# Performance work log

Measured on AMD Instinct MI355X. Metric: run time of the kernel, lower is better.

The kernel has to match this reference:

```python
import jax, jax.numpy as jnp
import numpy as np

B, T = 64, 512
IN, OUT, H = 256, 256, 1024


def _lstm_cell(x, h, c, Wih, Whh, bih, bhh):
    # PyTorch LSTMCell: gates = x@Wih^T + bih + h@Whh^T + bhh, order i,f,g,o
    gates = x @ Wih.T + bih + h @ Whh.T + bhh
    i, f, g, o = jnp.split(gates, 4, axis=-1)
    c_new = jax.nn.sigmoid(f) * c + jax.nn.sigmoid(i) * jnp.tanh(g)
    h_new = jax.nn.sigmoid(o) * jnp.tanh(c_new)
    return h_new, c_new


def setup_inputs() -> dict:
    key = jax.random.key(0)
    ks = jax.random.split(key, 12)
    s = 1.0 / np.sqrt(H)  # torch default uniform(-1/sqrt(H), 1/sqrt(H))
    u = lambda k, shp: jax.random.uniform(k, shp, jnp.float32, -s, s)
    return {
        "z": jax.random.normal(ks[0], (B, H), jnp.float32),
        "x": jax.random.normal(ks[1], (B, T, IN), jnp.float32),
        "Wih0": u(ks[2], (4 * H, IN)),
        "Whh0": u(ks[3], (4 * H, H)),
        "bih0": u(ks[4], (4 * H,)),
        "bhh0": u(ks[5], (4 * H,)),
        "Wih1": u(ks[6], (4 * H, H)),
        "Whh1": u(ks[7], (4 * H, H)),
        "bih1": u(ks[8], (4 * H,)),
        "bhh1": u(ks[9], (4 * H,)),
        "Wlin": u(ks[10], (OUT, H)),
        "blin": u(ks[11], (OUT,)),
    }


def reference(z, x, Wih0, Whh0, bih0, bhh0, Wih1, Whh1, bih1, bhh1, Wlin, blin):
    # Teacher-forcing unroll: h_t[l] init to z, c_t[l] init to 0, first input is zeros,
    # then input at step t+1 is x[:, t].
    x_tb = jnp.swapaxes(x, 0, 1)  # [T, B, IN]
    c0_init = jnp.zeros_like(z)

    def step(carry, x_t):
        cur_in, h0, c0, h1, c1 = carry
        h0, c0 = _lstm_cell(cur_in, h0, c0, Wih0, Whh0, bih0, bhh0)
        h1, c1 = _lstm_cell(h0, h1, c1, Wih1, Whh1, bih1, bhh1)
        out_t = h1 @ Wlin.T + blin  # [B, OUT]
        return (x_t, h0, c0, h1, c1), out_t

    init = (jnp.zeros((z.shape[0], Wih0.shape[1]), z.dtype), z, c0_init, z, c0_init)
    _, outs = jax.lax.scan(step, init, x_tb)  # outs: [T, B, OUT]
    return jnp.swapaxes(outs, 0, 1)  # [B, T, OUT]
```

## Files before the change

kernel.cpp:

```cpp
#include <hip/hip_runtime.h>
#include <hip/hip_bf16.h>
#include <math.h>


typedef __attribute__((ext_vector_type(8))) short bf16x8;
typedef __attribute__((ext_vector_type(4))) float f32x4;
typedef unsigned long long u64;

__device__ __forceinline__ float sigm(float v) { return 1.f / (1.f + expf(-v)); }

__device__ __forceinline__ unsigned short bf16_bits(float v) {
  __hip_bfloat16 hb = __float2bfloat16(v);
  unsigned short us;
  __builtin_memcpy(&us, &hb, 2);
  return us;
}

__device__ __forceinline__ void vstore_bf16(__hip_bfloat16* p, float v) {
  *(volatile unsigned short*)p = bf16_bits(v);
}


__global__ __launch_bounds__(256) void prep_w0(const float* __restrict__ Wih0,
                                               const float* __restrict__ Whh0,
                                               __hip_bfloat16* __restrict__ W0) {
  const unsigned n = 4096u * 1280u;
  for (unsigned d = blockIdx.x * blockDim.x + threadIdx.x; d < n;
       d += blockDim.x * gridDim.x) {
    unsigned r = d / 1280u;
    unsigned k = d - r * 1280u;
    unsigned u = r >> 2, g = r & 3u;
    unsigned srow = g * 1024u + u;
    float v = (k < 256u) ? Wih0[(size_t)srow * 256u + k]
                         : Whh0[(size_t)srow * 1024u + (k - 256u)];
    W0[d] = __float2bfloat16(v);
  }
}

__global__ __launch_bounds__(256) void prep_w1(const float* __restrict__ Wih1,
                                               const float* __restrict__ Whh1,
                                               const float* __restrict__ Wlin,
                                               __hip_bfloat16* __restrict__ W1) {
  const unsigned n = 4352u * 2048u;
  for (unsigned d = blockIdx.x * blockDim.x + threadIdx.x; d < n;
       d += blockDim.x * gridDim.x) {
    unsigned r = d >> 11;
    unsigned k = d & 2047u;
    float v;
    if (r < 4096u) {
      unsigned u = r >> 2, g = r & 3u;
      unsigned srow = g * 1024u + u;
      v = (k < 1024u) ? Wih1[(size_t)srow * 1024u + k]
                      : Whh1[(size_t)srow * 1024u + (k - 1024u)];
    } else {
      unsigned o = r - 4096u;
      v = (k < 1024u) ? 0.f : Wlin[(size_t)o * 1024u + (k - 1024u)];
    }
    W1[d] = __float2bfloat16(v);
  }
}

__global__ __launch_bounds__(256) void prep_x(const float* __restrict__ x,
                                              __hip_bfloat16* __restrict__ xbf) {
  const unsigned n = 512u * 64u * 256u;
  for (unsigned d = blockIdx.x * blockDim.x + threadIdx.x; d < n;
       d += blockDim.x * gridDim.x) {
    unsigned t = d >> 14;
    unsigned b = (d >> 8) & 63u;
    unsigned k = d & 255u;
    float v = (t == 0u) ? 0.f : x[((size_t)b * 512u + (t - 1u)) * 256u + k];
    xbf[d] = __float2bfloat16(v);
  }
}

__global__ __launch_bounds__(256) void prep_misc(
    const float* __restrict__ bih0, const float* __restrict__ bhh0,
    const float* __restrict__ bih1, const float* __restrict__ bhh1,
    const float* __restrict__ z, float* __restrict__ b0, float* __restrict__ b1,
    __hip_bfloat16* __restrict__ h0buf, __hip_bfloat16* __restrict__ h1buf) {
  for (int i = blockIdx.x * blockDim.x + threadIdx.x; i < 73728;
       i += blockDim.x * gridDim.x) {
    if (i < 4096) {
      int u = i >> 2, g = i & 3;
      b0[i] = bih0[g * 1024 + u] + bhh0[g * 1024 + u];
    } else if (i < 8192) {
      int r = i - 4096;
      int u = r >> 2, g = r & 3;
      b1[r] = bih1[g * 1024 + u] + bhh1[g * 1024 + u];
    } else {
      int j = i - 8192;
      float zv = z[j];
      vstore_bf16(h0buf + j, zv);
      vstore_bf16(h1buf + 2 * 65536 + j, zv);
    }
  }
}


__device__ __forceinline__ void do_proj(const __hip_bfloat16* __restrict__ h1p,
                                        const bf16x8* wp, float (*red)[16][68],
                                        const float* __restrict__ blin,
                                        float* __restrict__ out, int pcol,
                                        int pbat, int t_out, int tid, int w,
                                        int col, int kq) {
  f32x4 a0 = {0.f, 0.f, 0.f, 0.f};
  const __hip_bfloat16* ab =
      h1p + ((size_t)((pbat << 4) + col) << 10) + (w << 7) + (kq << 3);
#pragma unroll
  for (int c = 0; c < 4; ++c) {
    bf16x8 f = *(const bf16x8*)(ab + (c << 5));
    a0 = __builtin_amdgcn_mfma_f32_16x16x32_bf16(f, wp[c], a0, 0, 0, 0);
  }
  *(f32x4*)&red[w][col][(kq << 2)] = a0;
  __syncthreads();
  if (tid < 256) {
    int o_l = tid & 15, b = tid >> 4;
    float v = blin[(pcol << 4) + o_l];
#pragma unroll
    for (int ww = 0; ww < 8; ++ww) v += red[ww][o_l][b];
    out[(((size_t)((pbat << 4) + b) << 9) + (size_t)t_out) * 256 + (pcol << 4) +
        o_l] = v;
  }
}


__global__ __launch_bounds__(512) void k_persist(
    const __hip_bfloat16* __restrict__ xbf, const __hip_bfloat16* __restrict__ W0,
    const __hip_bfloat16* __restrict__ W1, const float* __restrict__ b0,
    const float* __restrict__ b1, const float* __restrict__ blin,
    __hip_bfloat16* __restrict__ h0buf, __hip_bfloat16* __restrict__ h1buf,
    float* __restrict__ out, unsigned* __restrict__ flags) {
  const int tid = threadIdx.x;
  const int lane = tid & 63;
  const int w = tid >> 6;
  const int bid = blockIdx.x;
  const int cb = bid << 4;
  const int col = lane & 15;
  const int kq = lane >> 4;
  const int n = cb + col;
  const bool isproj = (bid < 64);
  const int pcol = bid & 15;
  const int pbat = (bid >> 4) & 3;

  __shared__ int s_lead;
  {
    unsigned* lead = flags + 256;
    if (tid == 0) {
      unsigned xcc = 0;
      asm volatile("s_getreg_b32 %0, hwreg(HW_REG_XCC_ID)" : "=s"(xcc));
      unsigned old = __hip_atomic_fetch_add(&lead[xcc & 7u], 1u,
                                            __ATOMIC_RELAXED,
                                            __HIP_MEMORY_SCOPE_AGENT);
      s_lead = (old == 0u || bid < 8) ? 1 : 0;
    }
  }

  bf16x8 wa[5], wb[8], wp[4];
  {
    const __hip_bfloat16* p = W0 + (size_t)n * 1280 + w * 160 + (kq << 3);
#pragma unroll
    for (int c = 0; c < 5; ++c) wa[c] = *(const bf16x8*)(p + (c << 5));
  }
  {
    const __hip_bfloat16* p = W1 + ((size_t)n << 11) + (w << 8) + (kq << 3);
#pragma unroll
    for (int c = 0; c < 8; ++c) wb[c] = *(const bf16x8*)(p + (c << 5));
  }
  if (isproj) {
    const __hip_bfloat16* p = W1 +
        ((size_t)(4096 + (pcol << 4) + col) << 11) + 1024 + (w << 7) + (kq << 3);
#pragma unroll
    for (int c = 0; c < 4; ++c) wp[c] = *(const bf16x8*)(p + (c << 5));
  }

  const int u_l = tid & 3, bq = tid >> 2;
  float bias0[4], bias1[4];
  if (tid < 256) {
#pragma unroll
    for (int g = 0; g < 4; ++g) {
      bias0[g] = b0[cb + (u_l << 2) + g];
      bias1[g] = b1[cb + (u_l << 2) + g];
    }
  }
  float c0v = 0.f, c1v = 0.f;

  __shared__ float red[8][16][68];
  __shared__ unsigned short hst0[64][4];
  __shared__ unsigned short hst1[64][4];

  __syncthreads();

  for (int t = 0; t < 512; ++t) {
    const __hip_bfloat16* h0prev = h0buf + ((size_t)(t & 1) << 16);
    const __hip_bfloat16* h0cur = h0buf + ((size_t)((t + 1) & 1) << 16);
    const __hip_bfloat16* h1prev = h1buf + ((size_t)((t + 2) % 3) << 16);

    {
      f32x4 a0 = {0.f, 0.f, 0.f, 0.f}, a1 = a0, a2 = a0, a3 = a0;
#pragma unroll
      for (int c = 0; c < 5; ++c) {
        const int k0 = w * 160 + (c << 5);
        const __hip_bfloat16* ab;
        size_t rs;
        if (k0 < 256) {
          ab = xbf + ((size_t)t << 14) + k0 + (kq << 3);
          rs = 256;
        } else {
          ab = h0prev + (k0 - 256) + (kq << 3);
          rs = 1024;
        }
        bf16x8 f0 = *(const bf16x8*)(ab + (size_t)col * rs);
        bf16x8 f1 = *(const bf16x8*)(ab + (size_t)(16 + col) * rs);
        bf16x8 f2 = *(const bf16x8*)(ab + (size_t)(32 + col) * rs);
        bf16x8 f3 = *(const bf16x8*)(ab + (size_t)(48 + col) * rs);
        a0 = __builtin_amdgcn_mfma_f32_16x16x32_bf16(f0, wa[c], a0, 0, 0, 0);
        a1 = __builtin_amdgcn_mfma_f32_16x16x32_bf16(f1, wa[c], a1, 0, 0, 0);
        a2 = __builtin_amdgcn_mfma_f32_16x16x32_bf16(f2, wa[c], a2, 0, 0, 0);
        a3 = __builtin_amdgcn_mfma_f32_16x16x32_bf16(f3, wa[c], a3, 0, 0, 0);
      }
      *(f32x4*)&red[w][col][(kq << 2)] = a0;
      *(f32x4*)&red[w][col][16 + (kq << 2)] = a1;
      *(f32x4*)&red[w][col][32 + (kq << 2)] = a2;
      *(f32x4*)&red[w][col][48 + (kq << 2)] = a3;
    }
    __syncthreads();
    if (tid < 256) {
      float gg[4];
#pragma unroll
      for (int g = 0; g < 4; ++g) {
        float v = bias0[g];
#pragma unroll
        for (int ww = 0; ww < 8; ++ww) v += red[ww][(u_l << 2) + g][bq];
        gg[g] = v;
      }
      float cn = sigm(gg[1]) * c0v + sigm(gg[0]) * tanhf(gg[2]);
      c0v = cn;
      hst0[bq][u_l] = bf16_bits(sigm(gg[3]) * tanhf(cn));
    }
    __syncthreads();

    if (w == 0) {
      __builtin_amdgcn_s_waitcnt(0);
      if (s_lead) {
        __builtin_amdgcn_fence(__ATOMIC_ACQUIRE, "agent");
      } else {
        __builtin_amdgcn_sched_barrier(0);
        asm volatile("buffer_inv" ::: "memory");
        __builtin_amdgcn_sched_barrier(0);
      }
      u64 v0;
      __builtin_memcpy(&v0, &hst0[lane][0], 8);
      __hip_atomic_store((u64*)(h0buf + (((size_t)((t + 1) & 1)) << 16) +
                                ((size_t)lane << 10) + (cb >> 2)),
                         v0, __ATOMIC_RELAXED, __HIP_MEMORY_SCOPE_AGENT);
      if (t > 0) {
        u64 v1;
        __builtin_memcpy(&v1, &hst1[lane][0], 8);
        __hip_atomic_store((u64*)(h1buf + (((size_t)((t + 2) % 3)) << 16) +
                                  ((size_t)lane << 10) + (cb >> 2)),
                           v1, __ATOMIC_RELAXED, __HIP_MEMORY_SCOPE_AGENT);
      }
      __builtin_amdgcn_s_waitcnt(0);
      __builtin_amdgcn_sched_barrier(0);
      if (lane == 0)
        __hip_atomic_store(&flags[bid], (unsigned)(t + 1), __ATOMIC_RELAXED,
                           __HIP_MEMORY_SCOPE_AGENT);
    }

    if (isproj && t >= 2)
      do_proj(h1buf + (((size_t)((t + 1) % 3)) << 16), wp, red, blin, out,
              pcol, pbat, t - 2, tid, w, col, kq);

    if (w == 0) {
      const unsigned tgt = (unsigned)(t + 1);
      const u64* fq = (const u64*)flags;
      for (;;) {
        u64 q0 = __hip_atomic_load(&fq[2 * lane], __ATOMIC_RELAXED,
                                   __HIP_MEMORY_SCOPE_AGENT);
        u64 q1 = __hip_atomic_load(&fq[2 * lane + 1], __ATOMIC_RELAXED,
                                   __HIP_MEMORY_SCOPE_AGENT);
        int ok = ((unsigned)q0 >= tgt) & ((unsigned)(q0 >> 32) >= tgt) &
                 ((unsigned)q1 >= tgt) & ((unsigned)(q1 >> 32) >= tgt);
        if (__all(ok)) break;
        __builtin_amdgcn_s_sleep(1);
      }
    }
    __syncthreads();

    {
      const __hip_bfloat16* ab =
          ((w < 4) ? h0cur : h1prev) + ((w & 3) << 8) + (kq << 3);
      f32x4 a0 = {0.f, 0.f, 0.f, 0.f}, a1 = a0, a2 = a0, a3 = a0;
#pragma unroll
      for (int c = 0; c < 8; ++c) {
        const __hip_bfloat16* p = ab + (c << 5);
        bf16x8 f0 = *(const bf16x8*)(p + ((size_t)col << 10));
        bf16x8 f1 = *(const bf16x8*)(p + ((size_t)(16 + col) << 10));
        bf16x8 f2 = *(const bf16x8*)(p + ((size_t)(32 + col) << 10));
        bf16x8 f3 = *(const bf16x8*)(p + ((size_t)(48 + col) << 10));
        a0 = __builtin_amdgcn_mfma_f32_16x16x32_bf16(f0, wb[c], a0, 0, 0, 0);
        a1 = __builtin_amdgcn_mfma_f32_16x16x32_bf16(f1, wb[c], a1, 0, 0, 0);
        a2 = __builtin_amdgcn_mfma_f32_16x16x32_bf16(f2, wb[c], a2, 0, 0, 0);
        a3 = __builtin_amdgcn_mfma_f32_16x16x32_bf16(f3, wb[c], a3, 0, 0, 0);
      }
      *(f32x4*)&red[w][col][(kq << 2)] = a0;
      *(f32x4*)&red[w][col][16 + (kq << 2)] = a1;
      *(f32x4*)&red[w][col][32 + (kq << 2)] = a2;
      *(f32x4*)&red[w][col][48 + (kq << 2)] = a3;
    }
    __syncthreads();
    if (tid < 256) {
      float gg[4];
#pragma unroll
      for (int g = 0; g < 4; ++g) {
        float v = bias1[g];
#pragma unroll
        for (int ww = 0; ww < 8; ++ww) v += red[ww][(u_l << 2) + g][bq];
        gg[g] = v;
      }
      float cn = sigm(gg[1]) * c1v + sigm(gg[0]) * tanhf(gg[2]);
      c1v = cn;
      hst1[bq][u_l] = bf16_bits(sigm(gg[3]) * tanhf(cn));
    }
    __syncthreads();
  }

  if (isproj)
    do_proj(h1buf, wp, red, blin, out, pcol, pbat, 510, tid, w, col, kq);

  if (w == 0) {
    u64 v1;
    __builtin_memcpy(&v1, &hst1[lane][0], 8);
    __hip_atomic_store((u64*)(h1buf + ((size_t)3 << 16) +
                              ((size_t)lane << 10) + (cb >> 2)),
                       v1, __ATOMIC_RELAXED, __HIP_MEMORY_SCOPE_AGENT);
    __builtin_amdgcn_s_waitcnt(0);
    __builtin_amdgcn_sched_barrier(0);
    if (lane == 0)
      __hip_atomic_store(&flags[bid], 513u, __ATOMIC_RELAXED,
                         __HIP_MEMORY_SCOPE_AGENT);
  }
  if (!isproj) return;
  if (w == 0) {
    const u64* fq = (const u64*)flags;
    for (;;) {
      u64 q0 = __hip_atomic_load(&fq[2 * lane], __ATOMIC_RELAXED,
                                 __HIP_MEMORY_SCOPE_AGENT);
      u64 q1 = __hip_atomic_load(&fq[2 * lane + 1], __ATOMIC_RELAXED,
                                 __HIP_MEMORY_SCOPE_AGENT);
      int ok = ((unsigned)q0 >= 513u) & ((unsigned)(q0 >> 32) >= 513u) &
               ((unsigned)q1 >= 513u) & ((unsigned)(q1 >> 32) >= 513u);
      if (__all(ok)) break;
      __builtin_amdgcn_s_sleep(1);
    }
    __builtin_amdgcn_fence(__ATOMIC_ACQUIRE, "agent");
  }
  __syncthreads();
  do_proj(h1buf + ((size_t)3 << 16), wp, red, blin, out, pcol, pbat, 511, tid,
          w, col, kq);
}


extern "C" void kernel_launch(void* const* d_in, const int* in_sizes, int n_in,
                              void* d_out, int out_size, void* d_ws, size_t ws_size,
                              hipStream_t stream) {
  const float* z = (const float*)d_in[0];
  const float* x = (const float*)d_in[1];
  const float* Wih0 = (const float*)d_in[2];
  const float* Whh0 = (const float*)d_in[3];
  const float* bih0 = (const float*)d_in[4];
  const float* bhh0 = (const float*)d_in[5];
  const float* Wih1 = (const float*)d_in[6];
  const float* Whh1 = (const float*)d_in[7];
  const float* bih1 = (const float*)d_in[8];
  const float* bhh1 = (const float*)d_in[9];
  const float* Wlin = (const float*)d_in[10];
  const float* blin = (const float*)d_in[11];
  float* out = (float*)d_out;

  char* ws = (char*)d_ws;
  __hip_bfloat16* W0 = (__hip_bfloat16*)(ws);
  __hip_bfloat16* W1 = (__hip_bfloat16*)(ws + 10485760);
  __hip_bfloat16* xbf = (__hip_bfloat16*)(ws + 28311552);
  float* b0 = (float*)(ws + 45088768);
  float* b1 = (float*)(ws + 45105152);
  __hip_bfloat16* h0buf = (__hip_bfloat16*)(ws + 45121536);
  __hip_bfloat16* h1buf = (__hip_bfloat16*)(ws + 45383680);
  unsigned* flags = (unsigned*)(ws + 45907968);

  hipMemsetAsync(flags, 0, 4096, stream);
  prep_w0<<<4096, 256, 0, stream>>>(Wih0, Whh0, W0);
  prep_w1<<<4096, 256, 0, stream>>>(Wih1, Whh1, Wlin, W1);
  prep_x<<<4096, 256, 0, stream>>>(x, xbf);
  prep_misc<<<288, 256, 0, stream>>>(bih0, bhh0, bih1, bhh1, z, b0, b1, h0buf,
                                     h1buf);

  k_persist<<<256, 512, 0, stream>>>(xbf, W0, W1, b0, b1, blin, h0buf, h1buf,
                                     out, flags);
}
```

Measured before the change: 9.461 ms.

## Store hidden states directly to global and restructure per-step publish/sync

Gate threads now write their bf16 hidden outputs straight to global memory instead of staging them in shared memory and having wave 0 publish them with 64-bit atomics. The flag is published by thread 0 after a block-wide waitcnt and barrier, and the h1 ring shrinks to three slots with a reordered tail projection. Non-projection blocks prefetch the next step's x slice, the projection blocks move to bids 64-127, and the leader selection changes. Fast exp-based sigmoid and tanh replace expf and tanhf, trading some accuracy for cheaper activations, and the extra barriers add risk.

Result: no change. 9.436 ms (-0.3%).

```diff
diff --git a/kernel.cpp b/kernel.cpp
--- a/kernel.cpp
+++ b/kernel.cpp
@@ -7,7 +7,12 @@
 typedef __attribute__((ext_vector_type(4))) float f32x4;
 typedef unsigned long long u64;
 
-__device__ __forceinline__ float sigm(float v) { return 1.f / (1.f + expf(-v)); }
+__device__ __forceinline__ float sigm(float v) {
+  return 1.f / (1.f + __expf(-v));
+}
+__device__ __forceinline__ float ftanh(float v) {
+  return 2.f / (1.f + __expf(-2.f * v)) - 1.f;
+}
 
 __device__ __forceinline__ unsigned short bf16_bits(float v) {
   __hip_bfloat16 hb = __float2bfloat16(v);
@@ -138,7 +143,7 @@
   const int col = lane & 15;
   const int kq = lane >> 4;
   const int n = cb + col;
-  const bool isproj = (bid < 64);
+  const bool isproj = (bid >= 64 && bid < 128);
   const int pcol = bid & 15;
   const int pbat = (bid >> 4) & 3;
 
@@ -151,7 +156,7 @@
       unsigned old = __hip_atomic_fetch_add(&lead[xcc & 7u], 1u,
                                             __ATOMIC_RELAXED,
                                             __HIP_MEMORY_SCOPE_AGENT);
-      s_lead = (old == 0u || bid < 8) ? 1 : 0;
+      s_lead = (old == 0u || bid >= 248) ? 1 : 0;
     }
   }
 
@@ -185,8 +190,6 @@
   float c0v = 0.f, c1v = 0.f;
 
   __shared__ float red[8][16][68];
-  __shared__ unsigned short hst0[64][4];
-  __shared__ unsigned short hst1[64][4];
 
   __syncthreads();
 
@@ -233,44 +236,42 @@
         for (int ww = 0; ww < 8; ++ww) v += red[ww][(u_l << 2) + g][bq];
         gg[g] = v;
       }
-      float cn = sigm(gg[1]) * c0v + sigm(gg[0]) * tanhf(gg[2]);
+      float cn = sigm(gg[1]) * c0v + sigm(gg[0]) * ftanh(gg[2]);
       c0v = cn;
-      hst0[bq][u_l] = bf16_bits(sigm(gg[3]) * tanhf(cn));
+      vstore_bf16((__hip_bfloat16*)h0cur + ((size_t)bq << 10) + (cb >> 2) + u_l,
+                  sigm(gg[3]) * ftanh(cn));
     }
     __syncthreads();
 
     if (w == 0) {
-      __builtin_amdgcn_s_waitcnt(0);
+      __builtin_amdgcn_sched_barrier(0);
       if (s_lead) {
         __builtin_amdgcn_fence(__ATOMIC_ACQUIRE, "agent");
       } else {
-        __builtin_amdgcn_sched_barrier(0);
         asm volatile("buffer_inv" ::: "memory");
-        __builtin_amdgcn_sched_barrier(0);
-      }
-      u64 v0;
-      __builtin_memcpy(&v0, &hst0[lane][0], 8);
-      __hip_atomic_store((u64*)(h0buf + (((size_t)((t + 1) & 1)) << 16) +
-                                ((size_t)lane << 10) + (cb >> 2)),
-                         v0, __ATOMIC_RELAXED, __HIP_MEMORY_SCOPE_AGENT);
-      if (t > 0) {
-        u64 v1;
-        __builtin_memcpy(&v1, &hst1[lane][0], 8);
-        __hip_atomic_store((u64*)(h1buf + (((size_t)((t + 2) % 3)) << 16) +
-                                  ((size_t)lane << 10) + (cb >> 2)),
-                           v1, __ATOMIC_RELAXED, __HIP_MEMORY_SCOPE_AGENT);
-      }
-      __builtin_amdgcn_s_waitcnt(0);
+      }
       __builtin_amdgcn_sched_barrier(0);
-      if (lane == 0)
-        __hip_atomic_store(&flags[bid], (unsigned)(t + 1), __ATOMIC_RELAXED,
-                           __HIP_MEMORY_SCOPE_AGENT);
-    }
-
-    if (isproj && t >= 2)
+    }
+    __syncthreads();
+
+    if (isproj && t >= 2) {
       do_proj(h1buf + (((size_t)((t + 1) % 3)) << 16), wp, red, blin, out,
               pcol, pbat, t - 2, tid, w, col, kq);
-
+    } else if (w < 2 && t < 511) {
+      const char* px = (const char*)(xbf + ((size_t)(t + 1) << 14));
+      const int idx = (w << 6) | lane;
+#pragma unroll
+      for (int i = 0; i < 4; ++i) {
+        unsigned v = *(const unsigned*)(px + ((idx + (i << 7)) << 6));
+        asm volatile("" ::"v"(v));
+      }
+    }
+
+    __builtin_amdgcn_s_waitcnt(0);
+    __syncthreads();
+    if (tid == 0)
+      __hip_atomic_store(&flags[bid], (unsigned)(t + 1), __ATOMIC_RELAXED,
+                         __HIP_MEMORY_SCOPE_AGENT);
     if (w == 0) {
       const unsigned tgt = (unsigned)(t + 1);
       const u64* fq = (const u64*)flags;
@@ -318,28 +319,20 @@
         for (int ww = 0; ww < 8; ++ww) v += red[ww][(u_l << 2) + g][bq];
         gg[g] = v;
       }
-      float cn = sigm(gg[1]) * c1v + sigm(gg[0]) * tanhf(gg[2]);
+      float cn = sigm(gg[1]) * c1v + sigm(gg[0]) * ftanh(gg[2]);
       c1v = cn;
-      hst1[bq][u_l] = bf16_bits(sigm(gg[3]) * tanhf(cn));
-    }
-    __syncthreads();
-  }
-
-  if (isproj)
-    do_proj(h1buf, wp, red, blin, out, pcol, pbat, 510, tid, w, col, kq);
-
-  if (w == 0) {
-    u64 v1;
-    __builtin_memcpy(&v1, &hst1[lane][0], 8);
-    __hip_atomic_store((u64*)(h1buf + ((size_t)3 << 16) +
-                              ((size_t)lane << 10) + (cb >> 2)),
-                       v1, __ATOMIC_RELAXED, __HIP_MEMORY_SCOPE_AGENT);
-    __builtin_amdgcn_s_waitcnt(0);
-    __builtin_amdgcn_sched_barrier(0);
-    if (lane == 0)
-      __hip_atomic_store(&flags[bid], 513u, __ATOMIC_RELAXED,
-                         __HIP_MEMORY_SCOPE_AGENT);
-  }
+      vstore_bf16(h1buf + ((size_t)(t % 3) << 16) + ((size_t)bq << 10) +
+                      (cb >> 2) + u_l,
+                  sigm(gg[3]) * ftanh(cn));
+    }
+    __syncthreads();
+  }
+
+  __builtin_amdgcn_s_waitcnt(0);
+  __syncthreads();
+  if (tid == 0)
+    __hip_atomic_store(&flags[bid], 513u, __ATOMIC_RELAXED,
+                       __HIP_MEMORY_SCOPE_AGENT);
   if (!isproj) return;
   if (w == 0) {
     const u64* fq = (const u64*)flags;
@@ -356,7 +349,9 @@
     __builtin_amdgcn_fence(__ATOMIC_ACQUIRE, "agent");
   }
   __syncthreads();
-  do_proj(h1buf + ((size_t)3 << 16), wp, red, blin, out, pcol, pbat, 511, tid,
+  do_proj(h1buf, wp, red, blin, out, pcol, pbat, 510, tid, w, col, kq);
+  __syncthreads();
+  do_proj(h1buf + ((size_t)1 << 16), wp, red, blin, out, pcol, pbat, 511, tid,
           w, col, kq);
 }
 
@@ -386,7 +381,7 @@
   float* b1 = (float*)(ws + 45105152);
   __hip_bfloat16* h0buf = (__hip_bfloat16*)(ws + 45121536);
   __hip_bfloat16* h1buf = (__hip_bfloat16*)(ws + 45383680);
-  unsigned* flags = (unsigned*)(ws + 45907968);
+  unsigned* flags = (unsigned*)(ws + 45776896);
 
   hipMemsetAsync(flags, 0, 4096, stream);
   prep_w0<<<4096, 256, 0, stream>>>(Wih0, Whh0, W0);
```
